# Optimization experiments

Measured on AMD Instinct MI355X. Metric: run time of the kernel, lower is better.

## Reference

```python
import jax, jax.numpy as jnp
import numpy as np

L, H, P = 16384, 256, 512


def setup_inputs() -> dict:
    key = jax.random.key(0)
    ks = jax.random.split(key, 7)
    return {
        "input_sequence": jax.random.normal(ks[0], (L, H), jnp.float32),
        "A_diag": jax.random.normal(ks[1], (P,), jnp.float32) * 2.0,
        "G_diag": jax.random.uniform(ks[2], (P,), jnp.float32),  # in [0,1): keeps 1 - sigmoid(dt)*G > 0
        "dt": jax.random.normal(ks[3], (P,), jnp.float32) * 0.5,
        "B": jax.random.uniform(ks[4], (P, H, 2), jnp.float32, -1.0, 1.0) / np.sqrt(H).astype(np.float32),
        "C": jax.random.uniform(ks[5], (H, P, 2), jnp.float32, -1.0, 1.0) / np.sqrt(P).astype(np.float32),
        "D": jax.random.normal(ks[6], (H,), jnp.float32),
    }


def _combine(q_i, q_j):
    # q = (A, b); A: (..., 4, P) real 2x2 block-diagonal entries [A,B,C,D], b: (..., 2, P) complex
    A_i, b_i = q_i
    A_j, b_j = q_j
    iA, iB, iC, iD = A_i[..., 0, :], A_i[..., 1, :], A_i[..., 2, :], A_i[..., 3, :]
    jA, jB, jC, jD = A_j[..., 0, :], A_j[..., 1, :], A_j[..., 2, :], A_j[..., 3, :]
    A_new = jnp.stack(
        [jA * iA + jB * iC, jA * iB + jB * iD, jC * iA + jD * iC, jC * iB + jD * iD],
        axis=-2,
    )
    b1, b2 = b_i[..., 0, :], b_i[..., 1, :]
    b_new = jnp.stack([jA * b1 + jB * b2, jC * b1 + jD * b2], axis=-2) + b_j
    return (A_new, b_new)


def reference(input_sequence, A_diag, G_diag, dt, B, C, D):
    # complex parameter assembly
    B_c = B[..., 0] + 1j * B[..., 1]      # (P, H) complex
    C_c = C[..., 0] + 1j * C[..., 1]      # (H, P) complex

    # _soft_project_AGdt
    dts = jax.nn.sigmoid(dt)
    G = jax.nn.relu(G_diag)
    root = jnp.sqrt(1.0 - dts * G)
    denom = jnp.maximum(dts ** 2, 1e-6)
    A_low = (2.0 - dts * G - 2.0 * root) / denom
    A_high = (2.0 - dts * G + 2.0 * root) / denom
    A = A_low + jax.nn.relu(A_diag - A_low) - jax.nn.relu(A_diag - A_high)

    # Bu_k = B_complex @ u_k for all k: (L, P) complex64
    Bu = input_sequence.astype(B_c.dtype) @ B_c.T

    # IMEX2 transition matrix (diagonal 2x2 blocks), constant over time
    M = jnp.stack(
        [1.0 - dts * G, -dts * A, dts * (1.0 - dts * G), 1.0 - dts ** 2 * A],
        axis=0,
    )  # (4, P)
    seq_len = input_sequence.shape[0]
    M_el = jnp.broadcast_to(M, (seq_len, 4, M.shape[-1]))          # (L, 4, P)
    F = jnp.stack([dts * Bu, dts ** 2 * Bu], axis=1)               # (L, 2, P) complex

    _, xs = jax.lax.associative_scan(_combine, (M_el, F))
    ys = xs[:, 1, :]                                                # x-component, (L, P) complex

    out = (ys @ C_c.T).real.astype(input_sequence.dtype) + input_sequence * D
    return out
```

## Files before the change

### kernel.cpp

```cpp
#include <hip/hip_runtime.h>
#include <math.h>

#define L_SEQ 16384
#define H_DIM 256
#define P_DIM 512
#define CL 32
#define NC (L_SEQ / CL)

typedef __attribute__((ext_vector_type(8))) short bf16x8;
typedef __attribute__((ext_vector_type(4))) float f32x4;

static __device__ __forceinline__ unsigned short f2bf(float f) {
  unsigned int u = __builtin_bit_cast(unsigned int, f);
  u += 0x7FFFu + ((u >> 16) & 1u);
  return (unsigned short)(u >> 16);
}
static __device__ __forceinline__ float bflo(unsigned int v) {
  return __builtin_bit_cast(float, v << 16);
}
static __device__ __forceinline__ float bfhi(unsigned int v) {
  return __builtin_bit_cast(float, v & 0xFFFF0000u);
}
static __device__ __forceinline__ float bf2f(unsigned short s) {
  return __builtin_bit_cast(float, (unsigned int)s << 16);
}

__global__ __launch_bounds__(256) void prep_all(
    const float* __restrict__ A_diag, const float* __restrict__ G_diag,
    const float* __restrict__ dt, const float* __restrict__ B,
    const float* __restrict__ C, const float* __restrict__ u,
    float* __restrict__ prm, unsigned short* __restrict__ W1b,
    unsigned short* __restrict__ W2b, unsigned short* __restrict__ ub) {
  const int b = blockIdx.x;
  const int t = threadIdx.x;
  if (b < 2) {
    int p = b * 256 + t;
    float dts = 1.0f / (1.0f + expf(-dt[p]));
    float G = fmaxf(G_diag[p], 0.0f);
    float g = dts * G;
    float root = sqrtf(1.0f - g);
    float denom = fmaxf(dts * dts, 1e-6f);
    float A_low  = (2.0f - g - 2.0f * root) / denom;
    float A_high = (2.0f - g + 2.0f * root) / denom;
    float Ad = A_diag[p];
    float A = A_low + fmaxf(Ad - A_low, 0.0f) - fmaxf(Ad - A_high, 0.0f);
    float m00 = 1.0f - g;
    float m01 = -dts * A;
    float m10 = dts * (1.0f - g);
    float m11 = 1.0f - dts * dts * A;
    float c00 = m00, c01 = m01, c10 = m10, c11 = m11;
#pragma unroll
    for (int i = 0; i < 5; i++) {
      float n00 = c00 * c00 + c01 * c10;
      float n01 = c00 * c01 + c01 * c11;
      float n10 = c10 * c00 + c11 * c10;
      float n11 = c10 * c01 + c11 * c11;
      c00 = n00; c01 = n01; c10 = n10; c11 = n11;
    }
    prm[0 * P_DIM + p] = m00;
    prm[1 * P_DIM + p] = m01;
    prm[2 * P_DIM + p] = m10;
    prm[3 * P_DIM + p] = m11;
    prm[4 * P_DIM + p] = dts;
    prm[5 * P_DIM + p] = dts * dts;
    prm[6 * P_DIM + p] = c00;
    prm[7 * P_DIM + p] = c01;
    prm[8 * P_DIM + p] = c10;
    prm[9 * P_DIM + p] = c11;
  } else if (b < 2 + 1024) {
    int idx = (b - 2) * 256 + t;
    int n = idx >> 8;
    int k = idx & 255;
    int p = n >> 1, c = n & 1;
    W1b[idx] = f2bf(B[(p * H_DIM + k) * 2 + c]);
  } else if (b < 2 + 2048) {
    int idx = (b - 1026) * 256 + t;
    int h = idx >> 10;
    int k = idx & 1023;
    int p = k >> 1, c = k & 1;
    float v = C[(h * P_DIM + p) * 2 + c];
    W2b[idx] = f2bf(c ? -v : v);
  } else {
    int idx = (b - 2050) * 256 + t;
    float4 v = ((const float4*)u)[idx];
    ushort4 o;
    o.x = f2bf(v.x); o.y = f2bf(v.y); o.z = f2bf(v.z); o.w = f2bf(v.w);
    ((ushort4*)ub)[idx] = o;
  }
}

__global__ __launch_bounds__(256) void gemm1_scan(
    const unsigned short* __restrict__ A, const unsigned short* __restrict__ W,
    unsigned short* __restrict__ Out,
    const float* __restrict__ prm, float4* __restrict__ finals) {
  constexpr int BM = 128, BN = 128, N = 1024, K = H_DIM;
  __shared__ unsigned short tA[BM * 32];
  __shared__ unsigned short tW[BN * 32];
  __shared__ unsigned short stg[128 * 132];
  const int tid = threadIdx.x;
  const int lane = tid & 63;
  const int wid = tid >> 6;
  const int wr = wid >> 1;
  const int wc = wid & 1;
  const int bm = blockIdx.x * BM;
  const int bn = blockIdx.y * BN;

  f32x4 acc[4][4] = {};

  const int srow = lane >> 2;
  const int soff = (lane & 3) * 8;

  for (int k0 = 0; k0 < K; k0 += 32) {
    __syncthreads();
#pragma unroll
    for (int c = wid; c < BM / 16; c += 4) {
      const unsigned short* src = A + (size_t)(bm + c * 16 + srow) * K + k0 + soff;
      __builtin_amdgcn_global_load_lds(
          (const __attribute__((address_space(1))) void*)src,
          (__attribute__((address_space(3))) void*)(tA + c * 512), 16, 0, 0);
    }
#pragma unroll
    for (int c = wid; c < BN / 16; c += 4) {
      const unsigned short* src = W + (size_t)(bn + c * 16 + srow) * K + k0 + soff;
      __builtin_amdgcn_global_load_lds(
          (const __attribute__((address_space(1))) void*)src,
          (__attribute__((address_space(3))) void*)(tW + c * 512), 16, 0, 0);
    }
    __syncthreads();

    const int rA = lane & 15;
    const int kc = (lane >> 4) * 8;
    bf16x8 af[4], wf[4];
#pragma unroll
    for (int i = 0; i < 4; i++)
      af[i] = *(const bf16x8*)&tA[(wr * 64 + i * 16 + rA) * 32 + kc];
#pragma unroll
    for (int j = 0; j < 4; j++)
      wf[j] = *(const bf16x8*)&tW[(wc * 64 + j * 16 + rA) * 32 + kc];
#pragma unroll
    for (int i = 0; i < 4; i++)
#pragma unroll
      for (int j = 0; j < 4; j++)
        acc[i][j] = __builtin_amdgcn_mfma_f32_16x16x32_bf16(af[i], wf[j], acc[i][j], 0, 0, 0);
  }

  const int cr = (lane >> 4) * 4;
  const int cc = lane & 15;
#pragma unroll
  for (int i = 0; i < 4; i++)
#pragma unroll
    for (int j = 0; j < 4; j++) {
      const int rl = wr * 64 + i * 16 + cr;
      const int clc = wc * 64 + j * 16 + cc;
#pragma unroll
      for (int q = 0; q < 4; q++) {
        const unsigned short hv = f2bf(acc[i][j][q]);
        Out[(size_t)(bm + rl + q) * N + bn + clc] = hv;
        stg[(rl + q) * 132 + clc] = hv;
      }
    }

  __syncthreads();
  {
    const int i = tid >> 6;
    const int pl = tid & 63;
    const int p = (bn >> 1) + pl;
    const int cglob = blockIdx.x * 4 + i;
    float m00 = prm[0 * P_DIM + p], m01 = prm[1 * P_DIM + p];
    float m10 = prm[2 * P_DIM + p], m11 = prm[3 * P_DIM + p];
    float dts = prm[4 * P_DIM + p], dts2 = prm[5 * P_DIM + p];
    float x1r = 0.f, x2r = 0.f, x1i = 0.f, x2i = 0.f;
    const unsigned int* stg32 = (const unsigned int*)stg;
#pragma unroll 8
    for (int s = 0; s < CL; s++) {
      unsigned int v = stg32[(i * 32 + s) * 66 + pl];
      float bx = bflo(v), by = bfhi(v);
      float n1r = fmaf(m00, x1r, fmaf(m01, x2r, dts * bx));
      float n2r = fmaf(m10, x1r, fmaf(m11, x2r, dts2 * bx));
      float n1i = fmaf(m00, x1i, fmaf(m01, x2i, dts * by));
      float n2i = fmaf(m10, x1i, fmaf(m11, x2i, dts2 * by));
      x1r = n1r; x2r = n2r; x1i = n1i; x2i = n2i;
    }
    finals[(size_t)cglob * P_DIM + p] = make_float4(x1r, x2r, x1i, x2i);
  }
}

__global__ __launch_bounds__(NC) void scan_carry(
    const float4* __restrict__ finals, const float* __restrict__ prm,
    float4* __restrict__ carry) {
  int p = blockIdx.x;
  int c = threadIdx.x;
  __shared__ float4 sb[NC];
  float m00 = prm[6 * P_DIM + p], m01 = prm[7 * P_DIM + p];
  float m10 = prm[8 * P_DIM + p], m11 = prm[9 * P_DIM + p];
  float4 b = finals[c * P_DIM + p];
  for (int o = 1; o < NC; o <<= 1) {
    sb[c] = b;
    __syncthreads();
    float4 nb = (c >= o) ? sb[c - o] : make_float4(0.f, 0.f, 0.f, 0.f);
    __syncthreads();
    b.x = fmaf(m00, nb.x, fmaf(m01, nb.y, b.x));
    b.y = fmaf(m10, nb.x, fmaf(m11, nb.y, b.y));
    b.z = fmaf(m00, nb.z, fmaf(m01, nb.w, b.z));
    b.w = fmaf(m10, nb.z, fmaf(m11, nb.w, b.w));
    float n00 = m00 * m00 + m01 * m10;
    float n01 = m00 * m01 + m01 * m11;
    float n10 = m10 * m00 + m11 * m10;
    float n11 = m10 * m01 + m11 * m11;
    m00 = n00; m01 = n01; m10 = n10; m11 = n11;
  }
  if (c + 1 < NC) carry[(c + 1) * P_DIM + p] = b;
  if (c == 0) carry[p] = make_float4(0.f, 0.f, 0.f, 0.f);
}

__global__ __launch_bounds__(256) void gemm2_fused(
    const unsigned int* __restrict__ Bu16, const float* __restrict__ prm,
    const float4* __restrict__ carry, const unsigned short* __restrict__ W2b,
    const unsigned short* __restrict__ ub, const float* __restrict__ Dv,
    float* __restrict__ out) {
  __shared__ unsigned int yA[32 * 512];
  __shared__ unsigned short tW[256 * 32];
  const int tid = threadIdx.x;
  const int lane = tid & 63;
  const int wid = tid >> 6;
  const int row0 = blockIdx.x * 32;

#pragma unroll
  for (int h = 0; h < 2; h++) {
    const int p = tid + h * 256;
    float m00 = prm[0 * P_DIM + p], m01 = prm[1 * P_DIM + p];
    float m10 = prm[2 * P_DIM + p], m11 = prm[3 * P_DIM + p];
    float dts = prm[4 * P_DIM + p], dts2 = prm[5 * P_DIM + p];
    float4 s = carry[(size_t)blockIdx.x * P_DIM + p];
    float x1r = s.x, x2r = s.y, x1i = s.z, x2i = s.w;
    const unsigned int* src = Bu16 + (size_t)row0 * P_DIM + p;
#pragma unroll 8
    for (int i = 0; i < 32; i++) {
      unsigned int v = src[(size_t)i * P_DIM];
      float bx = bflo(v), by = bfhi(v);
      float n1r = fmaf(m00, x1r, fmaf(m01, x2r, dts * bx));
      float n2r = fmaf(m10, x1r, fmaf(m11, x2r, dts2 * bx));
      float n1i = fmaf(m00, x1i, fmaf(m01, x2i, dts * by));
      float n2i = fmaf(m10, x1i, fmaf(m11, x2i, dts2 * by));
      yA[(i * 512 + p) ^ ((i & 7) << 2)] =
          (unsigned int)f2bf(n2r) | ((unsigned int)f2bf(n2i) << 16);
      x1r = n1r; x2r = n2r; x1i = n1i; x2i = n2i;
    }
  }

  const int srow = lane >> 2;
  const int soff = (lane & 3) * 8;
  const int wr = wid >> 1;
  const int wc = wid & 1;
  const int rA = lane & 15;
  const int kc = (lane >> 4) * 8;
  const int arow = wr * 16 + rA;
  const unsigned short* yAs = (const unsigned short*)yA;
  f32x4 acc[8] = {};

  for (int k0 = 0; k0 < 1024; k0 += 32) {
    __syncthreads();
#pragma unroll
    for (int c = wid; c < 16; c += 4) {
      const unsigned short* src = W2b + (size_t)(c * 16 + srow) * 1024 + k0 + soff;
      __builtin_amdgcn_global_load_lds(
          (const __attribute__((address_space(1))) void*)src,
          (__attribute__((address_space(3))) void*)(tW + c * 512), 16, 0, 0);
    }
    __syncthreads();

    bf16x8 af = *(const bf16x8*)&yAs[((size_t)arow * 1024 + k0 + kc) ^ ((arow & 7) << 3)];
#pragma unroll
    for (int j = 0; j < 8; j++) {
      bf16x8 wf = *(const bf16x8*)&tW[(wc * 128 + j * 16 + rA) * 32 + kc];
      acc[j] = __builtin_amdgcn_mfma_f32_16x16x32_bf16(af, wf, acc[j], 0, 0, 0);
    }
  }

  const int cr = (lane >> 4) * 4;
  const int cc = lane & 15;
#pragma unroll
  for (int j = 0; j < 8; j++) {
    const int col = wc * 128 + j * 16 + cc;
    const float d = Dv[col];
#pragma unroll
    for (int q = 0; q < 4; q++) {
      const int row = row0 + wr * 16 + cr + q;
      const size_t idx = (size_t)row * H_DIM + col;
      out[idx] = fmaf(bf2f(ub[idx]), d, acc[j][q]);
    }
  }
}

extern "C" void kernel_launch(void* const* d_in, const int* in_sizes, int n_in,
                              void* d_out, int out_size, void* d_ws, size_t ws_size,
                              hipStream_t stream) {
  const float* u      = (const float*)d_in[0];
  const float* A_diag = (const float*)d_in[1];
  const float* G_diag = (const float*)d_in[2];
  const float* dt     = (const float*)d_in[3];
  const float* B      = (const float*)d_in[4];
  const float* C      = (const float*)d_in[5];
  const float* D      = (const float*)d_in[6];
  float* out = (float*)d_out;

  char* w = (char*)d_ws;
  unsigned short* Bu16 = (unsigned short*)w;
  unsigned short* ub   = (unsigned short*)(w + (size_t)L_SEQ * 1024 * 2);
  unsigned short* W1b  = ub + (size_t)L_SEQ * H_DIM;
  unsigned short* W2b  = W1b + 1024 * H_DIM;
  float* prm    = (float*)(W2b + H_DIM * 1024);
  float* finals = prm + 8192;
  float* carryb = finals + (size_t)NC * P_DIM * 4;

  prep_all<<<2 + 1024 + 1024 + 4096, 256, 0, stream>>>(
      A_diag, G_diag, dt, B, C, u, prm, W1b, W2b, ub);

  gemm1_scan<<<dim3(L_SEQ / 128, 1024 / 128), 256, 0, stream>>>(
      ub, W1b, Bu16, prm, (float4*)finals);

  scan_carry<<<P_DIM, NC, 0, stream>>>(
      (const float4*)finals, prm, (float4*)carryb);

  gemm2_fused<<<L_SEQ / 32, 256, 0, stream>>>(
      (const unsigned int*)Bu16, prm, (const float4*)carryb, W2b, ub, D, out);
}
```

Measured before the change: 74.69 us.

## Use k-group-major weight layouts and double-buffer W2 tiles in fused GEMM2

The bf16 weight matrices, and the shared-memory tiles that hold them, switch to a k-group-major layout ([k/8][n][8]) so that each 16-byte fragment load reads contiguous, conflict-free LDS rows. In gemm1, A-tile loads are re-indexed to match. In gemm2_fused, the scanned Y fragments are moved from LDS into 32 register vectors, and the freed LDS is reused as a double buffer for W2 tiles, so each k-step needs one barrier instead of two. The cost is much higher register pressure, which may spill, and a larger dynamic shared-memory allocation.

```diff
diff --git a/kernel.cpp b/kernel.cpp
--- a/kernel.cpp
+++ b/kernel.cpp
@@ -72,14 +72,14 @@
     int n = idx >> 8;
     int k = idx & 255;
     int p = n >> 1, c = n & 1;
-    W1b[idx] = f2bf(B[(p * H_DIM + k) * 2 + c]);
+    W1b[((size_t)(k >> 3) * 1024 + n) * 8 + (k & 7)] = f2bf(B[(p * H_DIM + k) * 2 + c]);
   } else if (b < 2 + 2048) {
     int idx = (b - 1026) * 256 + t;
     int h = idx >> 10;
     int k = idx & 1023;
     int p = k >> 1, c = k & 1;
     float v = C[(h * P_DIM + p) * 2 + c];
-    W2b[idx] = f2bf(c ? -v : v);
+    W2b[((size_t)(k >> 3) * 256 + h) * 8 + (k & 7)] = f2bf(c ? -v : v);
   } else {
     int idx = (b - 2050) * 256 + t;
     float4 v = ((const float4*)u)[idx];
@@ -93,50 +93,51 @@
     const unsigned short* __restrict__ A, const unsigned short* __restrict__ W,
     unsigned short* __restrict__ Out,
     const float* __restrict__ prm, float4* __restrict__ finals) {
-  constexpr int BM = 128, BN = 128, N = 1024, K = H_DIM;
-  __shared__ unsigned short tA[BM * 32];
-  __shared__ unsigned short tW[BN * 32];
+  constexpr int N = 1024, K = H_DIM;
+  __shared__ unsigned short tA[128 * 32];
+  __shared__ unsigned short tW[128 * 32];
   __shared__ unsigned short stg[128 * 132];
   const int tid = threadIdx.x;
   const int lane = tid & 63;
   const int wid = tid >> 6;
   const int wr = wid >> 1;
   const int wc = wid & 1;
-  const int bm = blockIdx.x * BM;
-  const int bn = blockIdx.y * BN;
+  const int bm = blockIdx.x * 128;
+  const int bn = blockIdx.y * 128;
 
   f32x4 acc[4][4] = {};
-
-  const int srow = lane >> 2;
-  const int soff = (lane & 3) * 8;
+  const int rA = lane & 15;
+  const int g = lane >> 4;
 
   for (int k0 = 0; k0 < K; k0 += 32) {
     __syncthreads();
 #pragma unroll
-    for (int c = wid; c < BM / 16; c += 4) {
-      const unsigned short* src = A + (size_t)(bm + c * 16 + srow) * K + k0 + soff;
+    for (int c = wid; c < 8; c += 4) {
+      const int unit = c * 64 + lane;
+      const int kg = unit >> 7, r = unit & 127;
+      const unsigned short* src = A + ((size_t)(bm + r) * 32 + (k0 >> 3) + kg) * 8;
       __builtin_amdgcn_global_load_lds(
           (const __attribute__((address_space(1))) void*)src,
           (__attribute__((address_space(3))) void*)(tA + c * 512), 16, 0, 0);
     }
 #pragma unroll
-    for (int c = wid; c < BN / 16; c += 4) {
-      const unsigned short* src = W + (size_t)(bn + c * 16 + srow) * K + k0 + soff;
+    for (int c = wid; c < 8; c += 4) {
+      const int unit = c * 64 + lane;
+      const int kg = unit >> 7, n = unit & 127;
+      const unsigned short* src = W + ((size_t)((k0 >> 3) + kg) * 1024 + bn + n) * 8;
       __builtin_amdgcn_global_load_lds(
           (const __attribute__((address_space(1))) void*)src,
           (__attribute__((address_space(3))) void*)(tW + c * 512), 16, 0, 0);
     }
     __syncthreads();
 
-    const int rA = lane & 15;
-    const int kc = (lane >> 4) * 8;
     bf16x8 af[4], wf[4];
 #pragma unroll
     for (int i = 0; i < 4; i++)
-      af[i] = *(const bf16x8*)&tA[(wr * 64 + i * 16 + rA) * 32 + kc];
+      af[i] = *(const bf16x8*)&tA[(g * 128 + wr * 64 + i * 16 + rA) * 8];
 #pragma unroll
     for (int j = 0; j < 4; j++)
-      wf[j] = *(const bf16x8*)&tW[(wc * 64 + j * 16 + rA) * 32 + kc];
+      wf[j] = *(const bf16x8*)&tW[(g * 128 + wc * 64 + j * 16 + rA) * 8];
 #pragma unroll
     for (int i = 0; i < 4; i++)
 #pragma unroll
@@ -218,8 +219,10 @@
     const float4* __restrict__ carry, const unsigned short* __restrict__ W2b,
     const unsigned short* __restrict__ ub, const float* __restrict__ Dv,
     float* __restrict__ out) {
-  __shared__ unsigned int yA[32 * 512];
-  __shared__ unsigned short tW[256 * 32];
+  extern __shared__ char smem[];
+  unsigned int* yA = (unsigned int*)smem;
+  unsigned short* tW0 = (unsigned short*)smem;
+  unsigned short* tW1 = (unsigned short*)(smem + 16384);
   const int tid = threadIdx.x;
   const int lane = tid & 63;
   const int wid = tid >> 6;
@@ -247,34 +250,45 @@
       x1r = n1r; x2r = n2r; x1i = n1i; x2i = n2i;
     }
   }
-
-  const int srow = lane >> 2;
-  const int soff = (lane & 3) * 8;
+  __syncthreads();
+
   const int wr = wid >> 1;
   const int wc = wid & 1;
   const int rA = lane & 15;
-  const int kc = (lane >> 4) * 8;
+  const int g = lane >> 4;
+  const int kc = g * 8;
   const int arow = wr * 16 + rA;
   const unsigned short* yAs = (const unsigned short*)yA;
-  f32x4 acc[8] = {};
-
-  for (int k0 = 0; k0 < 1024; k0 += 32) {
-    __syncthreads();
+  bf16x8 af[32];
+#pragma unroll
+  for (int t = 0; t < 32; t++)
+    af[t] = *(const bf16x8*)&yAs[((unsigned)(arow * 1024 + t * 32 + kc)) ^ ((arow & 7) << 3)];
+  __syncthreads();
+
+  auto STAGE = [&](unsigned short* buf, int k0) {
 #pragma unroll
     for (int c = wid; c < 16; c += 4) {
-      const unsigned short* src = W2b + (size_t)(c * 16 + srow) * 1024 + k0 + soff;
+      const unsigned short* src = W2b + ((size_t)(k0 >> 3) * 256 + c * 64 + lane) * 8;
       __builtin_amdgcn_global_load_lds(
           (const __attribute__((address_space(1))) void*)src,
-          (__attribute__((address_space(3))) void*)(tW + c * 512), 16, 0, 0);
-    }
-    __syncthreads();
-
-    bf16x8 af = *(const bf16x8*)&yAs[((size_t)arow * 1024 + k0 + kc) ^ ((arow & 7) << 3)];
+          (__attribute__((address_space(3))) void*)(buf + c * 512), 16, 0, 0);
+    }
+  };
+
+  f32x4 acc[8] = {};
+  STAGE(tW0, 0);
+  __syncthreads();
+#pragma unroll
+  for (int t = 0; t < 32; t++) {
+    const unsigned short* cur = (t & 1) ? tW1 : tW0;
+    unsigned short* nxt = (t & 1) ? tW0 : tW1;
+    if (t < 31) STAGE(nxt, (t + 1) * 32);
 #pragma unroll
     for (int j = 0; j < 8; j++) {
-      bf16x8 wf = *(const bf16x8*)&tW[(wc * 128 + j * 16 + rA) * 32 + kc];
-      acc[j] = __builtin_amdgcn_mfma_f32_16x16x32_bf16(af, wf, acc[j], 0, 0, 0);
-    }
+      bf16x8 wf = *(const bf16x8*)&cur[(g * 256 + wc * 128 + j * 16 + rA) * 8];
+      acc[j] = __builtin_amdgcn_mfma_f32_16x16x32_bf16(af[t], wf, acc[j], 0, 0, 0);
+    }
+    __syncthreads();
   }
 
   const int cr = (lane >> 4) * 4;
@@ -322,6 +336,6 @@
   scan_carry<<<P_DIM, NC, 0, stream>>>(
       (const float4*)finals, prm, (float4*)carryb);
 
-  gemm2_fused<<<L_SEQ / 32, 256, 0, stream>>>(
+  gemm2_fused<<<L_SEQ / 32, 256, 65536, stream>>>(
       (const unsigned int*)Bu16, prm, (const float4*)carryb, W2b, ub, D, out);
 }
```

Result: faster. 72.67 us (-2.7%).
